# Optimization experiments

Measured on AMD Instinct MI355X. Metric: run time of the kernel, lower is better.

## Reference

```python
import jax, jax.numpy as jnp
import numpy as np

K = 3
KK = K * K


def conv3x3(x, w, b):
    # x: [B,C,H,W], w: [O,C,3,3]
    y = jax.lax.conv_general_dilated(x, w, (1, 1), ((1, 1), (1, 1)),
                                     dimension_numbers=('NCHW', 'OIHW', 'NCHW'))
    return y + b[None, :, None, None]


def deform_conv(x, offset, w, b):
    # torchvision.ops.deform_conv2d, 3x3, pad=1, stride=1, no mask.
    B, C, H, W = x.shape
    off = offset.reshape(B, KK, 2, H, W)  # per kernel tap: (dy, dx)
    ky = jnp.repeat(jnp.arange(K, dtype=x.dtype) - 1, K)  # [9]
    kx = jnp.tile(jnp.arange(K, dtype=x.dtype) - 1, K)
    py = jnp.arange(H, dtype=x.dtype)[None, None, :, None] + ky[None, :, None, None] + off[:, :, 0]
    px = jnp.arange(W, dtype=x.dtype)[None, None, None, :] + kx[None, :, None, None] + off[:, :, 1]
    y0 = jnp.floor(py)
    x0 = jnp.floor(px)
    wy = (py - y0)[:, None]  # [B,1,9,H,W]
    wx = (px - x0)[:, None]
    y0i = y0.astype(jnp.int32)
    x0i = x0.astype(jnp.int32)
    xf = x.reshape(B, C, H * W)

    def corner(yi, xi):
        valid = ((yi >= 0) & (yi < H) & (xi >= 0) & (xi < W))
        idx = jnp.clip(yi, 0, H - 1) * W + jnp.clip(xi, 0, W - 1)  # [B,9,H,W]
        g = jax.vmap(lambda xb, ib: xb[:, ib.reshape(-1)])(xf, idx)  # [B,C,9*H*W]
        return g.reshape(B, C, KK, H, W) * valid[:, None].astype(x.dtype)

    val = (corner(y0i, x0i) * (1 - wy) * (1 - wx)
           + corner(y0i, x0i + 1) * (1 - wy) * wx
           + corner(y0i + 1, x0i) * wy * (1 - wx)
           + corner(y0i + 1, x0i + 1) * wy * wx)  # [B,C,9,H,W]
    out = jnp.einsum('bckhw,ock->bohw', val, w.reshape(w.shape[0], C, KK))
    return out + b[None, :, None, None]


def se_gate(x, w1, b1, w2, b2):
    # global avg pool -> 1x1 conv -> relu -> 1x1 conv -> sigmoid -> scale
    m = x.mean((2, 3))  # [B,C]
    h = jax.nn.relu(jnp.einsum('bc,rc->br', m, w1) + b1)
    g = jax.nn.sigmoid(jnp.einsum('br,cr->bc', h, w2) + b2)
    return x * g[:, :, None, None]


def resize_bilinear(x, oh, ow):
    # F.interpolate(mode='bilinear', align_corners=False)
    B, C, H, W = x.shape

    def coords(n_in, n_out):
        src = (jnp.arange(n_out, dtype=x.dtype) + 0.5) * (n_in / n_out) - 0.5
        src = jnp.clip(src, 0.0, n_in - 1)
        i0 = jnp.floor(src).astype(jnp.int32)
        i1 = jnp.minimum(i0 + 1, n_in - 1)
        return i0, i1, (src - i0).astype(x.dtype)

    y0, y1, wy = coords(H, oh)
    x = x[:, :, y0, :] * (1 - wy)[None, None, :, None] + x[:, :, y1, :] * wy[None, None, :, None]
    c0, c1, wc = coords(W, ow)
    x = x[:, :, :, c0] * (1 - wc)[None, None, None, :] + x[:, :, :, c1] * wc[None, None, None, :]
    return x


def setup_inputs() -> dict:
    key = jax.random.key(0)
    ks = jax.random.split(key, 12)
    B, C, H, W = 4, 64, 128, 128
    L, O, R = 4, 64, 4  # levels, out_channels, reduction=64//16
    d = {
        'x': jax.random.normal(ks[0], (B, C, H, W), jnp.float32),
        'off_w': jax.random.normal(ks[1], (L, 2 * KK, C, 3, 3), jnp.float32) * 0.01,
        'off_b': jax.random.normal(ks[2], (L, 2 * KK), jnp.float32) * 0.01,
        'dc_w': jax.random.normal(ks[3], (L, O, C, 3, 3), jnp.float32) * 0.05,
        'dc_b': jax.random.normal(ks[4], (L, O), jnp.float32) * 0.05,
        'se_w1': jax.random.normal(ks[5], (L, R, O), jnp.float32) * 0.1,
        'se_b1': jax.random.normal(ks[6], (L, R), jnp.float32) * 0.1,
        'se_w2': jax.random.normal(ks[7], (L, O, R), jnp.float32) * 0.1,
        'se_b2': jax.random.normal(ks[8], (L, O), jnp.float32) * 0.1,
        'fuse_w': jax.random.normal(ks[9], (O, L * O), jnp.float32) * 0.05,
        'fuse_b': jax.random.normal(ks[10], (O,), jnp.float32) * 0.05,
    }
    return d


def reference(x, off_w, off_b, dc_w, dc_b, se_w1, se_b1, se_w2, se_b2, fuse_w, fuse_b):
    B, _, H, W = x.shape
    L = off_w.shape[0]
    cur = x
    feats = []
    for i in range(L):
        if i > 0:
            cur = resize_bilinear(cur, cur.shape[2] // 2, cur.shape[3] // 2)
        off = conv3x3(cur, off_w[i], off_b[i])
        cur = deform_conv(cur, off, dc_w[i], dc_b[i])
        cur = se_gate(cur, se_w1[i], se_b1[i], se_w2[i], se_b2[i])
        feats.append(resize_bilinear(cur, H, W))
    for i in range(L - 2, -1, -1):
        feats[i] = feats[i] + feats[i + 1]
    fused = jnp.concatenate(feats, axis=1)  # [B, L*O, H, W]
    return jnp.einsum('bchw,oc->bohw', fused, fuse_w) + fuse_b[None, :, None, None]
```

## Files before the change

kernel.cpp:

```cpp
#include <hip/hip_runtime.h>
#include <hip/hip_bf16.h>
#include <math.h>


constexpr int Bn = 4;

typedef __attribute__((ext_vector_type(8))) short short8;
typedef __attribute__((ext_vector_type(4))) float f32x4;
typedef __attribute__((ext_vector_type(4))) unsigned uint4v;
typedef __attribute__((ext_vector_type(4))) unsigned short ushort4v;

static __device__ __forceinline__ short f2b(float f){
  union { float f; unsigned u; } v; v.f = f;
  unsigned r = v.u + 0x7fffu + ((v.u >> 16) & 1u);
  return (short)(r >> 16);
}
static __device__ __forceinline__ unsigned f2b2(float x, float y){
  union { __hip_bfloat162 h; unsigned u; } cv;
  cv.h = __float22bfloat162_rn(make_float2(x, y));
  return cv.u;
}
static __device__ __forceinline__ float blo(unsigned u){ return __uint_as_float(u << 16); }
static __device__ __forceinline__ float bhi(unsigned u){ return __uint_as_float(u & 0xffff0000u); }
static __device__ __forceinline__ void pinv(uint4v& x){ asm volatile("" : "+v"(x)); }

constexpr size_t OFF_CUR   = 0;
constexpr size_t OFF_DC    = OFF_CUR  + 4194304;
constexpr size_t OFF_T0    = OFF_DC   + 4194304;
constexpr size_t OFF_T1    = OFF_T0   + 4194304;
constexpr size_t OFF_T2    = OFF_T1   + 1048576;
constexpr size_t OFF_T3    = OFF_T2   + 262144;
constexpr size_t OFF_WSUMT = OFF_T3   + 65536;
constexpr size_t OFF_DCWT  = OFF_WSUMT + 8192;
constexpr size_t OFF_OWT   = OFF_DCWT  + 73728;
constexpr size_t OFF_SUMS  = OFF_OWT   + 36864;

__global__ void prep_k(const float* __restrict__ dc_w, const float* __restrict__ off_w,
                       const float* __restrict__ fuse_w, float* __restrict__ ws){
  int i = blockIdx.x * 256 + threadIdx.x;
  short* dcwT  = (short*)(ws + OFF_DCWT);
  short* owT   = (short*)(ws + OFF_OWT);
  short* wsumT = (short*)(ws + OFF_WSUMT);
  if (i < 147456){
    int oc = i / 576, r = i % 576, k = r >> 6, c = r & 63;
    dcwT[i] = f2b(dc_w[(oc*64 + c)*9 + k]);
  } else if (i < 147456 + 73728){
    int t = i - 147456;
    int lm = t / 576, l = lm >> 5, m = lm & 31, r = t % 576, k = r >> 6, c = r & 63;
    owT[t] = (m < 18) ? f2b(off_w[((l*18 + m)*64 + c)*9 + k]) : (short)0;
  } else if (i < 147456 + 73728 + 16384){
    int t = i - (147456 + 73728);
    int l = t / 4096, r = t % 4096, o = r / 64, c = r % 64;
    float s = 0.f;
    for (int jl = 0; jl <= l; jl++) s += fuse_w[o*256 + jl*64 + c];
    wsumT[t] = f2b(s);
  } else if (i < 147456 + 73728 + 16384 + 65536){
    ws[OFF_SUMS + (i - (147456 + 73728 + 16384))] = 0.f;
  }
}

__global__ __launch_bounds__(256) void cvt_k(const float* __restrict__ x, unsigned* __restrict__ cur){
  __shared__ float t[64][65];
  int tile = blockIdx.x;
  int b = tile >> 8, p0 = (tile & 255) << 6;
  int tx = threadIdx.x & 63, ty = threadIdx.x >> 6;
  #pragma unroll
  for (int c = ty; c < 64; c += 4)
    t[c][tx] = x[(((size_t)(b << 6) + c) << 14) + p0 + tx];
  __syncthreads();
  int u = threadIdx.x & 31, pr = threadIdx.x >> 5;
  #pragma unroll
  for (int i = 0; i < 8; i++){
    int pp = pr + i*8;
    unsigned v = f2b2(t[2*u][pp], t[2*u + 1][pp]);
    cur[((size_t)(b << 14) + p0 + pp)*32 + u] = v;
  }
}

template<int H, int LVL>
__global__ __launch_bounds__(256, 3) void deform_k(
    const unsigned* __restrict__ cur, const float* __restrict__ ws_all,
    const float* __restrict__ off_bias, const float* __restrict__ dc_bias,
    float* __restrict__ dc, float* __restrict__ sums){
  constexpr int W = H, P = H * W;
  constexpr int PITCHB = 584 * 2;
  constexpr int TPR8 = W/8, TPB8 = P/64;
  __shared__ __align__(16) short valA[16][584];
  __shared__ __align__(16) char  patchS[64*144];
  __shared__ __align__(16) float4 tapW[144];
  __shared__ __align__(8)  unsigned short tapIs[144][4];
  float* offsP = (float*)((char*)&valA[0][0] + 8192);
  const short* owt = (const short*)(ws_all + OFF_OWT) + LVL * 32 * 576;
  const short* dcw = (const short*)(ws_all + OFF_DCWT) + (size_t)LVL * 64 * 576;
  const int tid = threadIdx.x;
  const int wave = tid >> 6, lane = tid & 63;
  const int c0 = lane & 15, quad = lane >> 4, q4 = quad * 4;
  const int b = blockIdx.x / TPB8;
  const int rr = blockIdx.x % TPB8;
  const int hrow8 = (rr / TPR8) * 8, wcol8 = (rr % TPR8) * 8;
  const unsigned* curu = cur + (size_t)b * P * 32;

  uint4v wB[9];
  {
    const short* wrow = owt + ((wave & 1)*16 + c0)*576 + quad*8;
    #pragma unroll
    for (int kb = 0; kb < 9; kb++)
      wB[kb] = *(const uint4v*)&wrow[((wave >> 1)*9 + kb)*32];
    #pragma unroll
    for (int kb = 0; kb < 9; kb++) pinv(wB[kb]);
  }
  const int n = wave*16 + c0;
  uint4v wD[18];
  #pragma unroll
  for (int kb = 0; kb < 18; kb++)
    wD[kb] = *(const uint4v*)&dcw[n*576 + kb*32 + quad*8];
  #pragma unroll
  for (int kb = 0; kb < 18; kb++) pinv(wD[kb]);
  const float bt2 = dc_bias[LVL*64 + n];
  const int tk = tid % 9, tp = tid / 9;
  float oby = 0.f, obx = 0.f;
  if (tid < 144){
    oby = off_bias[LVL*18 + 2*tk];
    obx = off_bias[LVL*18 + 2*tk + 1];
  }
  const int pl = lane >> 3, cq = lane & 7;

  #pragma unroll 1
  for (int t = 0; t < 4; t++){
    const int srow = hrow8 + (t >> 1)*4, scol = wcol8 + (t & 1)*4;
    if (t) __syncthreads();

    #pragma unroll
    for (int i = 0; i < 2; i++){
      int pp = wave*16 + i*8 + pl;
      int R = pp >> 3, C = pp & 7;
      int yy = srow - 2 + R, xx = scol - 2 + C;
      bool v = ((unsigned)yy < (unsigned)H) & ((unsigned)xx < (unsigned)W);
      int idx = v ? (yy*W + xx) : 0;
      uint4 d = *(const uint4*)((const char*)curu + (size_t)idx*128 + cq*16);
      if (!v){ d.x = 0; d.y = 0; d.z = 0; d.w = 0; }
      *(uint4*)(patchS + pp*144 + cq*16) = d;
    }
    __syncthreads();

    {
      const int colw = wave & 1, kh = wave >> 1;
      const char* pb = patchS + (((c0 >> 2) + 1)*8 + (c0 & 3) + 1)*144 + quad*16;
      f32x4 oacc = {0,0,0,0};
      if (kh == 0){
        #pragma unroll
        for (int kb = 0; kb < 9; kb++){
          const int tap = kb >> 1;
          short8 a = *(const short8*)(pb + ((tap/3)*8 + (tap%3))*144 + (kb&1)*64);
          oacc = __builtin_amdgcn_mfma_f32_16x16x32_bf16(a, __builtin_bit_cast(short8, wB[kb]), oacc, 0, 0, 0);
        }
      } else {
        #pragma unroll
        for (int kb = 0; kb < 9; kb++){
          const int kk = 9 + kb, tap = kk >> 1;
          short8 a = *(const short8*)(pb + ((tap/3)*8 + (tap%3))*144 + (kk&1)*64);
          oacc = __builtin_amdgcn_mfma_f32_16x16x32_bf16(a, __builtin_bit_cast(short8, wB[kb]), oacc, 0, 0, 0);
        }
      }
      int comp = colw*16 + c0;
      if (comp < 18){
        #pragma unroll
        for (int r = 0; r < 4; r++) offsP[kh*288 + (q4 + r)*18 + comp] = oacc[r];
      }
    }
    __syncthreads();

    if (tid < 144){
      int p = tp, k = tk;
      int h = srow + (p >> 2), w = scol + (p & 3);
      float oy = offsP[p*18 + 2*k]     + offsP[288 + p*18 + 2*k]     + oby;
      float ox = offsP[p*18 + 2*k + 1] + offsP[288 + p*18 + 2*k + 1] + obx;
      float py = (float)(h + k/3 - 1) + oy;
      float px = (float)(w + k%3 - 1) + ox;
      float y0f = floorf(py), x0f = floorf(px);
      float fy = py - y0f, fx = px - x0f;
      int y0 = (int)y0f, x0 = (int)x0f, y1 = y0 + 1, x1 = x0 + 1;
      bool vy0 = (y0 >= 0) & (y0 < H), vy1 = (y1 >= 0) & (y1 < H);
      bool vx0 = (x0 >= 0) & (x0 < W), vx1 = (x1 >= 0) & (x1 < W);
      int y0c = min(max(y0, 0), H-1), y1c = min(max(y1, 0), H-1);
      int x0c = min(max(x0, 0), W-1), x1c = min(max(x1, 0), W-1);
      float gy = 1.f - fy, gx = 1.f - fx;
      tapW[tid] = make_float4((vy0 & vx0) ? gy*gx : 0.f,
                              (vy0 & vx1) ? gy*fx : 0.f,
                              (vy1 & vx0) ? fy*gx : 0.f,
                              (vy1 & vx1) ? fy*fx : 0.f);
      int ry = y0 - srow + 2, rx = x0 - scol + 2;
      if (((unsigned)ry < 7u) & ((unsigned)rx < 7u)){
        tapIs[tid][0] = (unsigned short)(0x8000u | (ry*8 + rx));
      } else {
        tapIs[tid][0] = (unsigned short)(y0c*W + x0c);
        tapIs[tid][1] = (unsigned short)(y0c*W + x1c);
        tapIs[tid][2] = (unsigned short)(y1c*W + x0c);
        tapIs[tid][3] = (unsigned short)(y1c*W + x1c);
      }
    }
    __syncthreads();

    {
      const char* curc8 = (const char*)curu + c0*8;
      int T = wave*36 + quad;
      int p = wave*4, k = quad;
      #pragma unroll
      for (int i = 0; i < 9; i++){
        float4 wv = tapW[T];
        unsigned short t0 = tapIs[T][0];
        uint2 u0, u1, u2, u3;
        if (t0 & 0x8000u){
          const char* pb2 = patchS + (int)(t0 & 0x7fffu)*144 + c0*8;
          u0 = *(const uint2*)(pb2);
          u1 = *(const uint2*)(pb2 + 144);
          u2 = *(const uint2*)(pb2 + 144*8);
          u3 = *(const uint2*)(pb2 + 144*9);
        } else {
          uint2 tw = *(const uint2*)tapIs[T];
          u0 = *(const uint2*)(curc8 + ((size_t)(tw.x & 0xffffu) << 7));
          u1 = *(const uint2*)(curc8 + ((size_t)(tw.x >> 16)     << 7));
          u2 = *(const uint2*)(curc8 + ((size_t)(tw.y & 0xffffu) << 7));
          u3 = *(const uint2*)(curc8 + ((size_t)(tw.y >> 16)     << 7));
        }
        float a0 = wv.x*blo(u0.x) + wv.y*blo(u1.x) + wv.z*blo(u2.x) + wv.w*blo(u3.x);
        float a1 = wv.x*bhi(u0.x) + wv.y*bhi(u1.x) + wv.z*bhi(u2.x) + wv.w*bhi(u3.x);
        float a2 = wv.x*blo(u0.y) + wv.y*blo(u1.y) + wv.z*blo(u2.y) + wv.w*blo(u3.y);
        float a3 = wv.x*bhi(u0.y) + wv.y*bhi(u1.y) + wv.z*bhi(u2.y) + wv.w*bhi(u3.y);
        uint2 pk; pk.x = f2b2(a0, a1); pk.y = f2b2(a2, a3);
        *(uint2*)((char*)&valA[0][0] + p*PITCHB + k*128 + c0*8) = pk;
        T += 4; k += 4; if (k >= 9){ k -= 9; ++p; }
      }
    }
    __syncthreads();

    f32x4 d0 = {bt2, bt2, bt2, bt2}, d1 = {0,0,0,0};
    #pragma unroll
    for (int kb = 0; kb < 9; kb++){
      short8 a = *(const short8*)&valA[c0][kb*32 + quad*8];
      d0 = __builtin_amdgcn_mfma_f32_16x16x32_bf16(a, __builtin_bit_cast(short8, wD[kb]), d0, 0, 0, 0);
    }
    #pragma unroll
    for (int kb = 9; kb < 18; kb++){
      short8 a = *(const short8*)&valA[c0][kb*32 + quad*8];
      d1 = __builtin_amdgcn_mfma_f32_16x16x32_bf16(a, __builtin_bit_cast(short8, wD[kb]), d1, 0, 0, 0);
    }
    f32x4 acc;
    #pragma unroll
    for (int r = 0; r < 4; r++) acc[r] = d0[r] + d1[r];
    float* dcb = dc + ((size_t)b*P + (size_t)(srow + quad)*W + scol)*64;
    #pragma unroll
    for (int r = 0; r < 4; r++) dcb[r*64 + n] = acc[r];
    float s = acc[0] + acc[1] + acc[2] + acc[3];
    s += __shfl_xor(s, 16);
    s += __shfl_xor(s, 32);
    if (quad == 0) atomicAdd(&sums[(LVL*16 + (blockIdx.x & 15))*256 + (b << 6) + n], s);
  }
}

template<int W, int LVL>
__global__ __launch_bounds__(256) void fuse_gd_k(
    const float* __restrict__ dcv, const float* __restrict__ sums,
    const float* __restrict__ se_w1, const float* __restrict__ se_b1,
    const float* __restrict__ se_w2, const float* __restrict__ se_b2,
    const float* __restrict__ ws_all, float* __restrict__ tmp, unsigned* __restrict__ curn){
  constexpr int P = W * W;
  constexpr bool POOL = (LVL < 3);
  constexpr float invP = 1.f / (float)P;
  __shared__ __align__(16) float fS[64][68];
  __shared__ __align__(16) float gsh[64];
  const short* wsl = (const short*)(ws_all + OFF_WSUMT) + LVL * 4096;
  const int tid = threadIdx.x, wave = tid >> 6, lane = tid & 63;
  const int c0 = lane & 15, quad = lane >> 4, q4 = quad * 4;
  int b, rp = 0, cs = 0;
  if (POOL){
    constexpr int tilesPerB = P / 64, tilesPerRow = W / 32;
    b = blockIdx.x / tilesPerB;
    int r = blockIdx.x % tilesPerB;
    rp = r / tilesPerRow; cs = r % tilesPerRow;
  } else {
    b = (blockIdx.x * 64) / P;
  }

  {
    int sg = tid >> 6, c = tid & 63;
    float part = 0.f;
    #pragma unroll
    for (int s = 0; s < 4; s++) part += sums[(LVL*16 + sg*4 + s)*256 + (b << 6) + c];
    fS[sg][c] = part;
    __syncthreads();
    if (tid < 64){
      int r = tid & 3, j = tid >> 2;
      float hp = 0.f;
      #pragma unroll
      for (int q = 0; q < 4; q++){
        int cq = j*4 + q;
        float m = (fS[0][cq] + fS[1][cq] + fS[2][cq] + fS[3][cq]) * invP;
        hp += m * se_w1[(LVL*4 + r)*64 + cq];
      }
      hp += __shfl_xor(hp, 4);  hp += __shfl_xor(hp, 8);
      hp += __shfl_xor(hp, 16); hp += __shfl_xor(hp, 32);
      float hr = fmaxf(hp + se_b1[LVL*4 + r], 0.f);
      float a = se_b2[LVL*64 + tid];
      #pragma unroll
      for (int r2 = 0; r2 < 4; r2++)
        a += __shfl(hr, r2) * se_w2[(LVL*64 + tid)*4 + r2];
      gsh[tid] = 1.f / (1.f + expf(-a));
    }
    __syncthreads();
  }

  float4 g4 = *(const float4*)&gsh[c0*4];
  #pragma unroll
  for (int i = 0; i < 4; i++){
    int lp = wave*16 + (lane >> 4) + i*4;
    size_t gpix = POOL ? ((size_t)b*P + (size_t)(2*rp + (lp >> 5))*W + cs*32 + (lp & 31))
                       : ((size_t)blockIdx.x*64 + lp);
    float4 d = *(const float4*)&dcv[gpix*64 + c0*4];
    float4 v = make_float4(d.x*g4.x, d.y*g4.y, d.z*g4.z, d.w*g4.w);
    *(float4*)&fS[lp][c0*4] = v;
  }
  __syncthreads();
  f32x4 acc[4] = {{0,0,0,0},{0,0,0,0},{0,0,0,0},{0,0,0,0}};
  #pragma unroll
  for (int kb = 0; kb < 2; kb++){
    float4 lo = *(const float4*)&fS[wave*16 + c0][kb*32 + quad*8];
    float4 hi = *(const float4*)&fS[wave*16 + c0][kb*32 + quad*8 + 4];
    uint4v ua = {f2b2(lo.x, lo.y), f2b2(lo.z, lo.w), f2b2(hi.x, hi.y), f2b2(hi.z, hi.w)};
    short8 a = __builtin_bit_cast(short8, ua);
    #pragma unroll
    for (int t = 0; t < 4; t++){
      short8 bf = *(const short8*)&wsl[(t*16 + c0)*64 + kb*32 + quad*8];
      acc[t] = __builtin_amdgcn_mfma_f32_16x16x32_bf16(a, bf, acc[t], 0, 0, 0);
    }
  }
  #pragma unroll
  for (int t = 0; t < 4; t++){
    int n = t*16 + c0;
    size_t plane = ((size_t)(b << 6) + n) * P;
    size_t pix = POOL ? ((size_t)(2*rp + (wave >> 1))*W + cs*32 + (wave & 1)*16 + q4)
                      : ((size_t)(blockIdx.x*64) - (size_t)b*P + wave*16 + q4);
    *(f32x4*)&tmp[plane + pix] = acc[t];
  }
  if constexpr (POOL){
    int j = tid >> 4, uu = tid & 15;
    float4 p0 = *(const float4*)&fS[2*j][uu*4];
    float4 p1 = *(const float4*)&fS[2*j + 1][uu*4];
    float4 p2 = *(const float4*)&fS[32 + 2*j][uu*4];
    float4 p3 = *(const float4*)&fS[33 + 2*j][uu*4];
    float4 av = make_float4(0.25f*(p0.x + p1.x + p2.x + p3.x),
                            0.25f*(p0.y + p1.y + p2.y + p3.y),
                            0.25f*(p0.z + p1.z + p2.z + p3.z),
                            0.25f*(p0.w + p1.w + p2.w + p3.w));
    uint2 pv = make_uint2(f2b2(av.x, av.y), f2b2(av.z, av.w));
    *(uint2*)&curn[((size_t)b*(P/4) + (size_t)rp*(W/2) + cs*16 + j)*32 + uu*2] = pv;
  }
}

__global__ void final_k(const float* __restrict__ ws_all, const float* __restrict__ fuse_bias,
                        float* __restrict__ out){
  int i = blockIdx.x * 256 + threadIdx.x;
  int w = i & 127, h = (i >> 7) & 127, o = (i >> 14) & 63, b = i >> 20;
  float acc = fuse_bias[o] + ws_all[OFF_T0 + (((size_t)(b << 6) + o) << 14) + (h << 7) + w];
  const float* tarr[3] = {ws_all + OFF_T1, ws_all + OFF_T2, ws_all + OFF_T3};
  #pragma unroll
  for (int li = 0; li < 3; li++){
    int l = li + 1, Hl = 128 >> l;
    float scale = 1.0f / (float)(1 << l);
    float sy = fminf(fmaxf((h + 0.5f)*scale - 0.5f, 0.f), (float)(Hl - 1));
    float sx = fminf(fmaxf((w + 0.5f)*scale - 0.5f, 0.f), (float)(Hl - 1));
    int y0 = (int)sy, x0 = (int)sx;
    float fy = sy - y0, fx = sx - x0;
    int y1 = min(y0 + 1, Hl - 1), x1 = min(x0 + 1, Hl - 1);
    const float* tb = tarr[li] + (size_t)((b << 6) + o) * Hl * Hl;
    float v00 = tb[y0*Hl + x0], v01 = tb[y0*Hl + x1];
    float v10 = tb[y1*Hl + x0], v11 = tb[y1*Hl + x1];
    acc += (1.f-fy)*((1.f-fx)*v00 + fx*v01) + fy*((1.f-fx)*v10 + fx*v11);
  }
  out[i] = acc;
}

extern "C" void kernel_launch(void* const* d_in, const int* in_sizes, int n_in,
                              void* d_out, int out_size, void* d_ws, size_t ws_size,
                              hipStream_t stream){
  (void)in_sizes; (void)n_in; (void)out_size; (void)ws_size;
  const float* x      = (const float*)d_in[0];
  const float* off_w  = (const float*)d_in[1];
  const float* off_b  = (const float*)d_in[2];
  const float* dc_w   = (const float*)d_in[3];
  const float* dc_b   = (const float*)d_in[4];
  const float* se_w1  = (const float*)d_in[5];
  const float* se_b1  = (const float*)d_in[6];
  const float* se_w2  = (const float*)d_in[7];
  const float* se_b2  = (const float*)d_in[8];
  const float* fuse_w = (const float*)d_in[9];
  const float* fuse_b = (const float*)d_in[10];
  float* out = (float*)d_out;
  float* ws = (float*)d_ws;
  unsigned* cur = (unsigned*)(ws + OFF_CUR);
  float* dc   = ws + OFF_DC;
  float* tmp[4] = {ws + OFF_T0, ws + OFF_T1, ws + OFF_T2, ws + OFF_T3};
  float* sums = ws + OFF_SUMS;

  prep_k<<<(303104 + 255)/256, 256, 0, stream>>>(dc_w, off_w, fuse_w, ws);
  cvt_k<<<1024, 256, 0, stream>>>(x, cur);

  deform_k<128,0><<<1024, 256, 0, stream>>>(cur, ws, off_b, dc_b, dc, sums);
  fuse_gd_k<128,0><<<1024, 256, 0, stream>>>(dc, sums, se_w1, se_b1, se_w2, se_b2, ws, tmp[0], cur);
  deform_k<64,1><<<256, 256, 0, stream>>>(cur, ws, off_b, dc_b, dc, sums);
  fuse_gd_k<64,1><<<256, 256, 0, stream>>>(dc, sums, se_w1, se_b1, se_w2, se_b2, ws, tmp[1], cur);
  deform_k<32,2><<<64, 256, 0, stream>>>(cur, ws, off_b, dc_b, dc, sums);
  fuse_gd_k<32,2><<<64, 256, 0, stream>>>(dc, sums, se_w1, se_b1, se_w2, se_b2, ws, tmp[2], cur);
  deform_k<16,3><<<16, 256, 0, stream>>>(cur, ws, off_b, dc_b, dc, sums);
  fuse_gd_k<16,3><<<16, 256, 0, stream>>>(dc, sums, se_w1, se_b1, se_w2, se_b2, ws, tmp[3], nullptr);

  final_k<<<16384, 256, 0, stream>>>(ws, fuse_b, out);
}
```

Baseline: 258.9 us.

## Use 16-pixel deform tiles for lower pyramid levels to raise block count

Adds a new deformable-conv kernel that processes a 4x4 pixel tile (16 pixels) per block instead of 64, with a smaller 6x6 halo patch, and launches it with four times as many blocks for levels 1-3. Level 0 keeps the original 64-pixel kernel. The aim is to fill the GPU at the small coarse levels where only 16-256 blocks were launched before. In exchange, weights are reread from global memory per block, the dc_w B-fragments are loaded per MFMA, and halo overhead per pixel is higher.

```diff
diff --git a/kernel.cpp b/kernel.cpp
--- a/kernel.cpp
+++ b/kernel.cpp
@@ -78,7 +78,7 @@
 }
 
 template<int H, int LVL>
-__global__ __launch_bounds__(256, 3) void deform_k(
+__global__ __launch_bounds__(256, 3) void deform8_k(
     const unsigned* __restrict__ cur, const float* __restrict__ ws_all,
     const float* __restrict__ off_bias, const float* __restrict__ dc_bias,
     float* __restrict__ dc, float* __restrict__ sums){
@@ -258,6 +258,151 @@
   }
 }
 
+template<int H, int LVL>
+__global__ __launch_bounds__(256, 7) void deform_k(
+    const unsigned* __restrict__ cur, const float* __restrict__ ws_all,
+    const float* __restrict__ off_bias, const float* __restrict__ dc_bias,
+    float* __restrict__ dc, float* __restrict__ sums){
+  constexpr int W = H, P = H * W;
+  constexpr int PITCHB = 584 * 2;
+  constexpr int TPR = W/4, TPB = P/16;
+  __shared__ __align__(16) short valA[16][584];
+  __shared__ __align__(16) float4 tapW[144];
+  __shared__ __align__(8)  unsigned short tapIs[144][4];
+  short* patch = &valA[0][0];
+  float* offsP = (float*)((char*)&valA[0][0] + 8192);
+  const short* owt = (const short*)(ws_all + OFF_OWT) + LVL * 32 * 576;
+  const short* dcw = (const short*)(ws_all + OFF_DCWT) + (size_t)LVL * 64 * 576;
+  const int tid = threadIdx.x;
+  const int wave = tid >> 6, lane = tid & 63;
+  const int c0 = lane & 15, quad = lane >> 4, q4 = quad * 4;
+  const int b = blockIdx.x / TPB;
+  const int rr = blockIdx.x % TPB;
+  const int hrow = (rr / TPR) * 4, wcol = (rr % TPR) * 4;
+  const unsigned* curu = cur + (size_t)b * P * 32;
+
+  {
+    #pragma unroll
+    for (int i = 0; i < 3; i++){
+      if (i < 2 || quad == 0){
+        int p36 = wave*9 + i*4 + quad;
+        int r6 = p36 / 6, c6 = p36 - r6*6;
+        int yy = hrow - 1 + r6, xx = wcol - 1 + c6;
+        bool v = ((unsigned)yy < (unsigned)H) & ((unsigned)xx < (unsigned)W);
+        int idx = v ? (yy*W + xx) : 0;
+        uint2 d = *(const uint2*)(curu + (size_t)idx*32 + c0*2);
+        if (!v){ d.x = 0u; d.y = 0u; }
+        *(uint2*)(patch + p36*72 + c0*4) = d;
+      }
+    }
+  }
+  __syncthreads();
+
+  {
+    const int colw = wave & 1, kh = wave >> 1;
+    const char* pb = (const char*)patch + ((c0 >> 2) * 6 + (c0 & 3)) * 144 + quad * 16;
+    const short* wrow = owt + (colw*16 + c0)*576 + quad*8;
+    f32x4 oacc = {0,0,0,0};
+    if (kh == 0){
+      #pragma unroll
+      for (int kb = 0; kb < 9; kb++){
+        const int tap = kb >> 1;
+        short8 a  = *(const short8*)(pb + ((tap/3)*864 + (tap%3)*144 + (kb&1)*64));
+        short8 bf = *(const short8*)&wrow[kb*32];
+        oacc = __builtin_amdgcn_mfma_f32_16x16x32_bf16(a, bf, oacc, 0, 0, 0);
+      }
+    } else {
+      #pragma unroll
+      for (int kb = 0; kb < 9; kb++){
+        const int kk = 9 + kb, tap = kk >> 1;
+        short8 a  = *(const short8*)(pb + ((tap/3)*864 + (tap%3)*144 + (kk&1)*64));
+        short8 bf = *(const short8*)&wrow[kk*32];
+        oacc = __builtin_amdgcn_mfma_f32_16x16x32_bf16(a, bf, oacc, 0, 0, 0);
+      }
+    }
+    int comp = colw*16 + c0;
+    if (comp < 18){
+      #pragma unroll
+      for (int r = 0; r < 4; r++) offsP[kh*288 + (q4 + r)*18 + comp] = oacc[r];
+    }
+  }
+  __syncthreads();
+
+  if (tid < 144){
+    int p = tid / 9, k = tid % 9;
+    int h = hrow + (p >> 2), w = wcol + (p & 3);
+    float oy = offsP[p*18 + 2*k]     + offsP[288 + p*18 + 2*k]     + off_bias[LVL*18 + 2*k];
+    float ox = offsP[p*18 + 2*k + 1] + offsP[288 + p*18 + 2*k + 1] + off_bias[LVL*18 + 2*k + 1];
+    float py = (float)(h + k/3 - 1) + oy;
+    float px = (float)(w + k%3 - 1) + ox;
+    float y0f = floorf(py), x0f = floorf(px);
+    float fy = py - y0f, fx = px - x0f;
+    int y0 = (int)y0f, x0 = (int)x0f, y1 = y0 + 1, x1 = x0 + 1;
+    bool vy0 = (y0 >= 0) & (y0 < H), vy1 = (y1 >= 0) & (y1 < H);
+    bool vx0 = (x0 >= 0) & (x0 < W), vx1 = (x1 >= 0) & (x1 < W);
+    int y0c = min(max(y0, 0), H-1), y1c = min(max(y1, 0), H-1);
+    int x0c = min(max(x0, 0), W-1), x1c = min(max(x1, 0), W-1);
+    float gy = 1.f - fy, gx = 1.f - fx;
+    tapW[tid] = make_float4((vy0 & vx0) ? gy*gx : 0.f,
+                            (vy0 & vx1) ? gy*fx : 0.f,
+                            (vy1 & vx0) ? fy*gx : 0.f,
+                            (vy1 & vx1) ? fy*fx : 0.f);
+    ushort4v ti = { (unsigned short)(y0c*W + x0c), (unsigned short)(y0c*W + x1c),
+                    (unsigned short)(y1c*W + x0c), (unsigned short)(y1c*W + x1c) };
+    *(ushort4v*)tapIs[tid] = ti;
+  }
+  __syncthreads();
+
+  {
+    const char* curc8 = (const char*)curu + c0*8;
+    int T = wave*36 + quad;
+    int p = T/9, k = T - p*9;
+    #pragma unroll
+    for (int i = 0; i < 9; i++){
+      float4 wv = tapW[T];
+      uint2 tw = *(const uint2*)tapIs[T];
+      uint2 u0 = *(const uint2*)(curc8 + ((size_t)(tw.x & 0xffffu) << 7));
+      uint2 u1 = *(const uint2*)(curc8 + ((size_t)(tw.x >> 16) << 7));
+      uint2 u2 = *(const uint2*)(curc8 + ((size_t)(tw.y & 0xffffu) << 7));
+      uint2 u3 = *(const uint2*)(curc8 + ((size_t)(tw.y >> 16) << 7));
+      float a0 = wv.x*blo(u0.x) + wv.y*blo(u1.x) + wv.z*blo(u2.x) + wv.w*blo(u3.x);
+      float a1 = wv.x*bhi(u0.x) + wv.y*bhi(u1.x) + wv.z*bhi(u2.x) + wv.w*bhi(u3.x);
+      float a2 = wv.x*blo(u0.y) + wv.y*blo(u1.y) + wv.z*blo(u2.y) + wv.w*blo(u3.y);
+      float a3 = wv.x*bhi(u0.y) + wv.y*bhi(u1.y) + wv.z*bhi(u2.y) + wv.w*bhi(u3.y);
+      uint2 pk; pk.x = f2b2(a0, a1); pk.y = f2b2(a2, a3);
+      *(uint2*)((char*)&valA[0][0] + p*PITCHB + k*128 + c0*8) = pk;
+      T += 4; k += 4; if (k >= 9){ k -= 9; ++p; }
+    }
+  }
+  __syncthreads();
+
+  const int n = wave*16 + c0;
+  float bt2 = dc_bias[LVL*64 + n];
+  f32x4 d0 = {bt2, bt2, bt2, bt2}, d1 = {0,0,0,0};
+  #pragma unroll
+  for (int kb = 0; kb < 9; kb++){
+    short8 a  = *(const short8*)&valA[c0][kb*32 + quad*8];
+    short8 bf = *(const short8*)&dcw[n*576 + kb*32 + quad*8];
+    d0 = __builtin_amdgcn_mfma_f32_16x16x32_bf16(a, bf, d0, 0, 0, 0);
+  }
+  #pragma unroll
+  for (int kb = 9; kb < 18; kb++){
+    short8 a  = *(const short8*)&valA[c0][kb*32 + quad*8];
+    short8 bf = *(const short8*)&dcw[n*576 + kb*32 + quad*8];
+    d1 = __builtin_amdgcn_mfma_f32_16x16x32_bf16(a, bf, d1, 0, 0, 0);
+  }
+  f32x4 acc;
+  #pragma unroll
+  for (int r = 0; r < 4; r++) acc[r] = d0[r] + d1[r];
+  float* dcb = dc + ((size_t)b*P + (size_t)(hrow + quad)*W + wcol)*64;
+  #pragma unroll
+  for (int r = 0; r < 4; r++) dcb[r*64 + n] = acc[r];
+  float s = acc[0] + acc[1] + acc[2] + acc[3];
+  s += __shfl_xor(s, 16);
+  s += __shfl_xor(s, 32);
+  if (quad == 0) atomicAdd(&sums[(LVL*16 + (blockIdx.x & 15))*256 + (b << 6) + n], s);
+}
+
 template<int W, int LVL>
 __global__ __launch_bounds__(256) void fuse_gd_k(
     const float* __restrict__ dcv, const float* __restrict__ sums,
@@ -405,13 +550,13 @@
   prep_k<<<(303104 + 255)/256, 256, 0, stream>>>(dc_w, off_w, fuse_w, ws);
   cvt_k<<<1024, 256, 0, stream>>>(x, cur);
 
-  deform_k<128,0><<<1024, 256, 0, stream>>>(cur, ws, off_b, dc_b, dc, sums);
+  deform8_k<128,0><<<1024, 256, 0, stream>>>(cur, ws, off_b, dc_b, dc, sums);
   fuse_gd_k<128,0><<<1024, 256, 0, stream>>>(dc, sums, se_w1, se_b1, se_w2, se_b2, ws, tmp[0], cur);
-  deform_k<64,1><<<256, 256, 0, stream>>>(cur, ws, off_b, dc_b, dc, sums);
+  deform_k<64,1><<<1024, 256, 0, stream>>>(cur, ws, off_b, dc_b, dc, sums);
   fuse_gd_k<64,1><<<256, 256, 0, stream>>>(dc, sums, se_w1, se_b1, se_w2, se_b2, ws, tmp[1], cur);
-  deform_k<32,2><<<64, 256, 0, stream>>>(cur, ws, off_b, dc_b, dc, sums);
+  deform_k<32,2><<<256, 256, 0, stream>>>(cur, ws, off_b, dc_b, dc, sums);
   fuse_gd_k<32,2><<<64, 256, 0, stream>>>(dc, sums, se_w1, se_b1, se_w2, se_b2, ws, tmp[2], cur);
-  deform_k<16,3><<<16, 256, 0, stream>>>(cur, ws, off_b, dc_b, dc, sums);
+  deform_k<16,3><<<64, 256, 0, stream>>>(cur, ws, off_b, dc_b, dc, sums);
   fuse_gd_k<16,3><<<16, 256, 0, stream>>>(dc, sums, se_w1, se_b1, se_w2, se_b2, ws, tmp[3], nullptr);
 
   final_k<<<16384, 256, 0, stream>>>(ws, fuse_b, out);
```

Result: faster. 228.5 us (-11.8%).
